# Kernel tuning notes

Hardware: AMD Instinct MI355X
Metric: run time of the kernel (lower is better)

## Reference

```python
import jax, jax.numpy as jnp
import numpy as np

FP8_MAX = 448.0  # torch.finfo(float8_e4m3fn).max


def quant_fp8(x):
    # dynamic per-tensor quantization: amax -> scale -> cast to fp8
    amax = jnp.max(jnp.abs(x)).astype(jnp.float32)
    scale = jnp.minimum(FP8_MAX / jnp.maximum(amax, 1e-12), FP8_MAX)
    x_fp8 = jnp.clip(x * scale, -FP8_MAX, FP8_MAX).astype(jnp.float8_e4m3fn)
    return x_fp8, 1.0 / scale  # (fp8 data, dequant scale)


def setup_inputs() -> dict:
    key = jax.random.key(0)
    k1, k2, k3 = jax.random.split(key, 3)
    B, S, IN, OUT = 4, 8192, 1024, 1024
    input = jax.random.normal(k1, (B, S, IN), dtype=jnp.float32)
    # kaiming_uniform_(a=sqrt(5)) -> uniform(-1/sqrt(in), 1/sqrt(in))
    bound = 1.0 / np.sqrt(IN)
    weight = jax.random.uniform(k2, (OUT, IN), dtype=jnp.float32, minval=-bound, maxval=bound)
    bias = jax.random.uniform(k3, (OUT,), dtype=jnp.float32, minval=-bound, maxval=bound)
    return {"input": input, "weight": weight, "bias": bias}


def reference(input, weight, bias):
    prev_shape = input.shape
    x2d = input.reshape(-1, weight.shape[1])  # [T, in]
    w_fp8, w_scale = quant_fp8(weight)
    x_fp8, x_scale = quant_fp8(x2d)
    # bias add, bf16 output
    acc = jnp.matmul(x_fp8.astype(jnp.float32), w_fp8.astype(jnp.float32).T)
    out2d = (acc * (x_scale * w_scale) + bias).astype(jnp.bfloat16)
    out = out2d.reshape(*prev_shape[:-1], weight.shape[0]).astype(input.dtype)
    return out
```

## Files before the change

kernel.cpp:

```cpp
#include <hip/hip_runtime.h>
#include <hip/hip_bf16.h>

typedef float f32x4 __attribute__((ext_vector_type(4)));
typedef long lx2 __attribute__((ext_vector_type(2)));

#define FP8_MAX_F 448.0f

__device__ __forceinline__ float wave_max(float m) {
#pragma unroll
    for (int off = 32; off > 0; off >>= 1)
        m = fmaxf(m, __shfl_xor(m, off));
    return m;
}

__global__ void amax2_kernel(const float* __restrict__ x, long nx,
                             const float* __restrict__ w, long nw,
                             float* __restrict__ px, float* __restrict__ pw,
                             int ga) {
    __shared__ float red[4];
    const float* src; long n; float* dst; int bid, blocks;
    if ((int)blockIdx.x < ga) { src = x; n = nx; dst = px; bid = blockIdx.x; blocks = ga; }
    else { src = w; n = nw; dst = pw; bid = blockIdx.x - ga; blocks = gridDim.x - ga; }

    const long stride = (long)blocks * blockDim.x * 16;
    long i = ((long)bid * blockDim.x + threadIdx.x) * 16;
    float m = 0.0f;
    for (; i < n; i += stride) {
        f32x4 v0 = *(const f32x4*)(src + i);
        f32x4 v1 = *(const f32x4*)(src + i + 4);
        f32x4 v2 = *(const f32x4*)(src + i + 8);
        f32x4 v3 = *(const f32x4*)(src + i + 12);
        float m0 = fmaxf(fmaxf(fabsf(v0.x), fabsf(v0.y)), fmaxf(fabsf(v0.z), fabsf(v0.w)));
        float m1 = fmaxf(fmaxf(fabsf(v1.x), fabsf(v1.y)), fmaxf(fabsf(v1.z), fabsf(v1.w)));
        float m2 = fmaxf(fmaxf(fabsf(v2.x), fabsf(v2.y)), fmaxf(fabsf(v2.z), fabsf(v2.w)));
        float m3 = fmaxf(fmaxf(fabsf(v3.x), fabsf(v3.y)), fmaxf(fabsf(v3.z), fabsf(v3.w)));
        m = fmaxf(m, fmaxf(fmaxf(m0, m1), fmaxf(m2, m3)));
    }
    m = wave_max(m);
    const int wave = threadIdx.x >> 6;
    if ((threadIdx.x & 63) == 0) red[wave] = m;
    __syncthreads();
    if (threadIdx.x == 0)
        dst[bid] = fmaxf(fmaxf(red[0], red[1]), fmaxf(red[2], red[3]));
}

__global__ void amax_final_kernel(const float* __restrict__ px, int npx,
                                  const float* __restrict__ pw, int npw,
                                  unsigned* __restrict__ amax) {
    __shared__ float red[4];
    const float* p; int n;
    if (blockIdx.x == 0) { p = px; n = npx; } else { p = pw; n = npw; }
    float m = 0.0f;
    for (int i = threadIdx.x; i < n; i += blockDim.x) m = fmaxf(m, p[i]);
    m = wave_max(m);
    const int wave = threadIdx.x >> 6;
    if ((threadIdx.x & 63) == 0) red[wave] = m;
    __syncthreads();
    if (threadIdx.x == 0) {
        m = fmaxf(fmaxf(red[0], red[1]), fmaxf(red[2], red[3]));
        amax[blockIdx.x] = __float_as_uint(m);
    }
}

__global__ void quant2_kernel(const float* __restrict__ x, long nx8,
                              const float* __restrict__ w, long nw8,
                              const unsigned* __restrict__ amax_bits,
                              unsigned* __restrict__ qx, unsigned* __restrict__ qw,
                              int ga) {
    const float* src; long n8; unsigned* q; int bid, blocks; float a;
    if ((int)blockIdx.x < ga) { src = x; n8 = nx8; q = qx; bid = blockIdx.x; blocks = ga;
                                a = __uint_as_float(amax_bits[0]); }
    else { src = w; n8 = nw8; q = qw; bid = blockIdx.x - ga; blocks = gridDim.x - ga;
           a = __uint_as_float(amax_bits[1]); }
    const float scale = fminf(FP8_MAX_F / fmaxf(a, 1e-12f), FP8_MAX_F);

    const long stride = (long)blocks * blockDim.x;
    for (long i = (long)bid * blockDim.x + threadIdx.x; i < n8; i += stride) {
        f32x4 v0 = *(const f32x4*)(src + i * 8);
        f32x4 v1 = *(const f32x4*)(src + i * 8 + 4);
        float c0 = fminf(fmaxf(v0.x * scale, -FP8_MAX_F), FP8_MAX_F);
        float c1 = fminf(fmaxf(v0.y * scale, -FP8_MAX_F), FP8_MAX_F);
        float c2 = fminf(fmaxf(v0.z * scale, -FP8_MAX_F), FP8_MAX_F);
        float c3 = fminf(fmaxf(v0.w * scale, -FP8_MAX_F), FP8_MAX_F);
        float c4 = fminf(fmaxf(v1.x * scale, -FP8_MAX_F), FP8_MAX_F);
        float c5 = fminf(fmaxf(v1.y * scale, -FP8_MAX_F), FP8_MAX_F);
        float c6 = fminf(fmaxf(v1.z * scale, -FP8_MAX_F), FP8_MAX_F);
        float c7 = fminf(fmaxf(v1.w * scale, -FP8_MAX_F), FP8_MAX_F);
        int r0 = __builtin_amdgcn_cvt_pk_fp8_f32(c0, c1, 0, false);
        r0 = __builtin_amdgcn_cvt_pk_fp8_f32(c2, c3, r0, true);
        int r1 = __builtin_amdgcn_cvt_pk_fp8_f32(c4, c5, 0, false);
        r1 = __builtin_amdgcn_cvt_pk_fp8_f32(c6, c7, r1, true);
        uint2 rr; rr.x = (unsigned)r0; rr.y = (unsigned)r1;
        *(uint2*)(q + i * 2) = rr;
    }
}

__global__ __launch_bounds__(512, 2) void gemm_fp8_kernel(
    const unsigned char* __restrict__ Xq,
    const unsigned char* __restrict__ Wq,
    const float* __restrict__ bias,
    const unsigned* __restrict__ amax_bits,
    float* __restrict__ out,
    int M, int N, int K, int nbn)
{
    __shared__ unsigned char ldsA[2][16384];
    __shared__ unsigned char ldsB[2][16384];

    const int tid  = threadIdx.x;
    const int lane = tid & 63;
    const int wave = tid >> 6;
    const int wm128 = (wave >> 2) * 128;
    const int wn64  = (wave & 3) * 64;

    const int l15 = lane & 15;
    const int lhi = lane >> 4;

    const int cpx = gridDim.x >> 3;
    const int wg  = ((int)blockIdx.x & 7) * cpx + ((int)blockIdx.x >> 3);
    const int bn = wg % nbn;
    const int bm = wg / nbn;
    const int rowStart = bm << 8;
    const int colStart = bn << 8;

    const int aoff0 = lhi * 4096 + (wm128 + l15) * 16;
    const int boff  = lhi * 4096 + (wn64 + l15) * 16;

    const int c0  = tid >> 8;
    const int rr_ = tid & 255;
    const size_t aoffs = (size_t)(rowStart + rr_) * K + c0 * 16;
    const size_t boffs = (size_t)(colStart + rr_) * K + c0 * 16;
    const int tid16 = tid * 16;

    f32x4 acc[8][4] = {};

#define STAGE(t, slot)                                                                          \
    do {                                                                                        \
        const size_t kk_ = (size_t)(t) * 64;                                                    \
        __builtin_amdgcn_global_load_lds(                                                       \
            (const __attribute__((address_space(1))) void*)(Xq + aoffs + kk_),                  \
            (__attribute__((address_space(3))) void*)(&ldsA[slot][tid16]), 16, 0, 0);           \
        __builtin_amdgcn_global_load_lds(                                                       \
            (const __attribute__((address_space(1))) void*)(Xq + aoffs + 32 + kk_),             \
            (__attribute__((address_space(3))) void*)(&ldsA[slot][8192 + tid16]), 16, 0, 0);    \
        __builtin_amdgcn_global_load_lds(                                                       \
            (const __attribute__((address_space(1))) void*)(Wq + boffs + kk_),                  \
            (__attribute__((address_space(3))) void*)(&ldsB[slot][tid16]), 16, 0, 0);           \
        __builtin_amdgcn_global_load_lds(                                                       \
            (const __attribute__((address_space(1))) void*)(Wq + boffs + 32 + kk_),             \
            (__attribute__((address_space(3))) void*)(&ldsB[slot][8192 + tid16]), 16, 0, 0);    \
    } while (0)

#define TILE(slot, STG)                                                                         \
    do {                                                                                        \
        asm volatile("s_waitcnt vmcnt(0)" ::: "memory");                                        \
        __builtin_amdgcn_s_barrier();                                                           \
        __builtin_amdgcn_sched_barrier(0);                                                      \
        lx2 af[4], bf[4];                                                                       \
        _Pragma("unroll")                                                                       \
        for (int q_ = 0; q_ < 4; ++q_) {                                                        \
            bf[q_] = *(const lx2*)(&ldsB[slot][boff + q_ * 256]);                               \
            af[q_] = *(const lx2*)(&ldsA[slot][aoff0 + q_ * 256]);                              \
        }                                                                                       \
        STG;                                                                                    \
        asm volatile("s_waitcnt lgkmcnt(0)" ::: "memory");                                      \
        __builtin_amdgcn_sched_barrier(0);                                                      \
        __builtin_amdgcn_s_setprio(1);                                                          \
        _Pragma("unroll")                                                                       \
        for (int ks_ = 0; ks_ < 2; ++ks_)                                                       \
            _Pragma("unroll")                                                                   \
            for (int mi_ = 0; mi_ < 4; ++mi_)                                                   \
                _Pragma("unroll")                                                               \
                for (int ni_ = 0; ni_ < 4; ++ni_)                                               \
                    acc[mi_][ni_] = __builtin_amdgcn_mfma_f32_16x16x32_fp8_fp8(                 \
                        af[mi_][ks_], bf[ni_][ks_], acc[mi_][ni_], 0, 0, 0);                    \
        __builtin_amdgcn_s_setprio(0);                                                          \
        __builtin_amdgcn_s_barrier();                                                           \
        __builtin_amdgcn_sched_barrier(0);                                                      \
        _Pragma("unroll")                                                                       \
        for (int q_ = 0; q_ < 4; ++q_)                                                          \
            af[q_] = *(const lx2*)(&ldsA[slot][aoff0 + 1024 + q_ * 256]);                       \
        asm volatile("s_waitcnt lgkmcnt(0)" ::: "memory");                                      \
        __builtin_amdgcn_sched_barrier(0);                                                      \
        __builtin_amdgcn_s_setprio(1);                                                          \
        _Pragma("unroll")                                                                       \
        for (int ks_ = 0; ks_ < 2; ++ks_)                                                       \
            _Pragma("unroll")                                                                   \
            for (int mi_ = 0; mi_ < 4; ++mi_)                                                   \
                _Pragma("unroll")                                                               \
                for (int ni_ = 0; ni_ < 4; ++ni_)                                               \
                    acc[4 + mi_][ni_] = __builtin_amdgcn_mfma_f32_16x16x32_fp8_fp8(             \
                        af[mi_][ks_], bf[ni_][ks_], acc[4 + mi_][ni_], 0, 0, 0);                \
        __builtin_amdgcn_s_setprio(0);                                                          \
    } while (0)

    STAGE(0, 0);

    const int nIter = K >> 7;
#pragma unroll 1
    for (int i = 0; i < nIter; ++i) {
        TILE(0, STAGE(2 * i + 1, 1));
        TILE(1, do { if (i < nIter - 1) STAGE(2 * i + 2, 0); } while (0));
    }
#undef TILE
#undef STAGE

    const float ax = __uint_as_float(amax_bits[0]);
    const float aw = __uint_as_float(amax_bits[1]);
    const float sx = fminf(FP8_MAX_F / fmaxf(ax, 1e-12f), FP8_MAX_F);
    const float sw = fminf(FP8_MAX_F / fmaxf(aw, 1e-12f), FP8_MAX_F);
    const float s  = (1.0f / sx) * (1.0f / sw);

    const int lhi4 = (lane >> 4) * 4;
#pragma unroll
    for (int ni = 0; ni < 4; ++ni) {
        const int col = colStart + wn64 + ni * 16 + l15;
        const float bv = bias[col];
#pragma unroll
        for (int mi = 0; mi < 8; ++mi) {
            const size_t rbase = (size_t)(rowStart + wm128 + mi * 16 + lhi4) * N + col;
#pragma unroll
            for (int j = 0; j < 4; ++j) {
                float t = acc[mi][ni][j] * s;
                t = t + bv;
                out[rbase + (size_t)j * N] = __bfloat162float(__float2bfloat16(t));
            }
        }
    }
}

extern "C" void kernel_launch(void* const* d_in, const int* in_sizes, int n_in,
                              void* d_out, int out_size, void* d_ws, size_t ws_size,
                              hipStream_t stream) {
    const float* input  = (const float*)d_in[0];
    const float* weight = (const float*)d_in[1];
    const float* bias   = (const float*)d_in[2];
    float* out = (float*)d_out;

    const int K = 1024;
    const int N = in_sizes[2];
    const long nX = in_sizes[0];
    const long nW = (long)N * K;
    const int M = (int)(nX / K);

    const int GA = 1984;
    const int GW = 64;

    unsigned char* ws = (unsigned char*)d_ws;
    unsigned* amax = (unsigned*)ws;
    unsigned char* Xq = ws + 256;
    unsigned char* Wq = Xq + (size_t)M * K;
    float* px = (float*)(Wq + (size_t)N * K);
    float* pw = px + GA;

    amax2_kernel<<<GA + GW, 256, 0, stream>>>(input, nX, weight, nW, px, pw, GA);
    amax_final_kernel<<<2, 256, 0, stream>>>(px, GA, pw, GW, amax);

    quant2_kernel<<<2048, 256, 0, stream>>>(input, nX / 8, weight, nW / 8, amax,
                                            (unsigned*)Xq, (unsigned*)Wq, GA);

    const int nbn = N / 256;
    const int nwg = (M / 256) * nbn;
    gemm_fp8_kernel<<<dim3(nwg), dim3(512), 0, stream>>>(Xq, Wq, bias, amax, out, M, N, K, nbn);
}
```

Before: 142.8 us.

## Shrink FP8 GEMM block tile to 256x128 and raise occupancy to four blocks

The GEMM block tile narrows from 256x256 to 256x128. Each of the 8 waves now computes a 64x64 sub-tile instead of 128x64, and the second MFMA half-step per K tile is removed. The B-side LDS buffer is halved, accumulators drop from 32 to 16 vectors, and launch bounds ask for 4 blocks per CU. This doubles the number of workgroups, aiming for more latency hiding and better load balance, at the cost of lower data reuse per block and more redundant loads of A from memory.

```diff
diff --git a/kernel.cpp b/kernel.cpp
--- a/kernel.cpp
+++ b/kernel.cpp
@@ -95,7 +95,7 @@
     }
 }
 
-__global__ __launch_bounds__(512, 2) void gemm_fp8_kernel(
+__global__ __launch_bounds__(512, 4) void gemm_fp8_kernel(
     const unsigned char* __restrict__ Xq,
     const unsigned char* __restrict__ Wq,
     const float* __restrict__ bias,
@@ -104,13 +104,13 @@
     int M, int N, int K, int nbn)
 {
     __shared__ unsigned char ldsA[2][16384];
-    __shared__ unsigned char ldsB[2][16384];
+    __shared__ unsigned char ldsB[2][8192];
 
     const int tid  = threadIdx.x;
     const int lane = tid & 63;
     const int wave = tid >> 6;
-    const int wm128 = (wave >> 2) * 128;
-    const int wn64  = (wave & 3) * 64;
+    const int wm64 = (wave >> 1) * 64;
+    const int wn64 = (wave & 1) * 64;
 
     const int l15 = lane & 15;
     const int lhi = lane >> 4;
@@ -120,18 +120,16 @@
     const int bn = wg % nbn;
     const int bm = wg / nbn;
     const int rowStart = bm << 8;
-    const int colStart = bn << 8;
-
-    const int aoff0 = lhi * 4096 + (wm128 + l15) * 16;
-    const int boff  = lhi * 4096 + (wn64 + l15) * 16;
-
-    const int c0  = tid >> 8;
-    const int rr_ = tid & 255;
-    const size_t aoffs = (size_t)(rowStart + rr_) * K + c0 * 16;
-    const size_t boffs = (size_t)(colStart + rr_) * K + c0 * 16;
+    const int colStart = bn << 7;
+
+    const int aoff = lhi * 4096 + (wm64 + l15) * 16;
+    const int boff = lhi * 2048 + (wn64 + l15) * 16;
+
+    const size_t aoffs = (size_t)(rowStart + (tid & 255)) * K + (tid >> 8) * 16;
+    const size_t boffs = (size_t)(colStart + (tid & 127)) * K + (tid >> 7) * 16;
     const int tid16 = tid * 16;
 
-    f32x4 acc[8][4] = {};
+    f32x4 acc[4][4] = {};
 
 #define STAGE(t, slot)                                                                          \
     do {                                                                                        \
@@ -145,9 +143,6 @@
         __builtin_amdgcn_global_load_lds(                                                       \
             (const __attribute__((address_space(1))) void*)(Wq + boffs + kk_),                  \
             (__attribute__((address_space(3))) void*)(&ldsB[slot][tid16]), 16, 0, 0);           \
-        __builtin_amdgcn_global_load_lds(                                                       \
-            (const __attribute__((address_space(1))) void*)(Wq + boffs + 32 + kk_),             \
-            (__attribute__((address_space(3))) void*)(&ldsB[slot][8192 + tid16]), 16, 0, 0);    \
     } while (0)
 
 #define TILE(slot, STG)                                                                         \
@@ -158,8 +153,8 @@
         lx2 af[4], bf[4];                                                                       \
         _Pragma("unroll")                                                                       \
         for (int q_ = 0; q_ < 4; ++q_) {                                                        \
+            af[q_] = *(const lx2*)(&ldsA[slot][aoff + q_ * 256]);                               \
             bf[q_] = *(const lx2*)(&ldsB[slot][boff + q_ * 256]);                               \
-            af[q_] = *(const lx2*)(&ldsA[slot][aoff0 + q_ * 256]);                              \
         }                                                                                       \
         STG;                                                                                    \
         asm volatile("s_waitcnt lgkmcnt(0)" ::: "memory");                                      \
@@ -174,23 +169,6 @@
                     acc[mi_][ni_] = __builtin_amdgcn_mfma_f32_16x16x32_fp8_fp8(                 \
                         af[mi_][ks_], bf[ni_][ks_], acc[mi_][ni_], 0, 0, 0);                    \
         __builtin_amdgcn_s_setprio(0);                                                          \
-        __builtin_amdgcn_s_barrier();                                                           \
-        __builtin_amdgcn_sched_barrier(0);                                                      \
-        _Pragma("unroll")                                                                       \
-        for (int q_ = 0; q_ < 4; ++q_)                                                          \
-            af[q_] = *(const lx2*)(&ldsA[slot][aoff0 + 1024 + q_ * 256]);                       \
-        asm volatile("s_waitcnt lgkmcnt(0)" ::: "memory");                                      \
-        __builtin_amdgcn_sched_barrier(0);                                                      \
-        __builtin_amdgcn_s_setprio(1);                                                          \
-        _Pragma("unroll")                                                                       \
-        for (int ks_ = 0; ks_ < 2; ++ks_)                                                       \
-            _Pragma("unroll")                                                                   \
-            for (int mi_ = 0; mi_ < 4; ++mi_)                                                   \
-                _Pragma("unroll")                                                               \
-                for (int ni_ = 0; ni_ < 4; ++ni_)                                               \
-                    acc[4 + mi_][ni_] = __builtin_amdgcn_mfma_f32_16x16x32_fp8_fp8(             \
-                        af[mi_][ks_], bf[ni_][ks_], acc[4 + mi_][ni_], 0, 0, 0);                \
-        __builtin_amdgcn_s_setprio(0);                                                          \
     } while (0)
 
     STAGE(0, 0);
@@ -210,14 +188,14 @@
     const float sw = fminf(FP8_MAX_F / fmaxf(aw, 1e-12f), FP8_MAX_F);
     const float s  = (1.0f / sx) * (1.0f / sw);
 
-    const int lhi4 = (lane >> 4) * 4;
+    const int lhi4 = lhi * 4;
 #pragma unroll
     for (int ni = 0; ni < 4; ++ni) {
         const int col = colStart + wn64 + ni * 16 + l15;
         const float bv = bias[col];
 #pragma unroll
-        for (int mi = 0; mi < 8; ++mi) {
-            const size_t rbase = (size_t)(rowStart + wm128 + mi * 16 + lhi4) * N + col;
+        for (int mi = 0; mi < 4; ++mi) {
+            const size_t rbase = (size_t)(rowStart + wm64 + mi * 16 + lhi4) * N + col;
 #pragma unroll
             for (int j = 0; j < 4; ++j) {
                 float t = acc[mi][ni][j] * s;
@@ -258,7 +236,7 @@
     quant2_kernel<<<2048, 256, 0, stream>>>(input, nX / 8, weight, nW / 8, amax,
                                             (unsigned*)Xq, (unsigned*)Wq, GA);
 
-    const int nbn = N / 256;
+    const int nbn = N / 128;
     const int nwg = (M / 256) * nbn;
     gemm_fp8_kernel<<<dim3(nwg), dim3(512), 0, stream>>>(Xq, Wq, bias, amax, out, M, N, K, nbn);
 }
```

After: 174.7 us. 22.4% more time.
